# Performance work log

Hardware: AMD Instinct MI355X
Metric: run time of the kernel (lower is better)

## Reference

```python
import jax, jax.numpy as jnp
import numpy as np

ALPHA_LIM = (float(np.exp(-1.0 / 5.0)), float(np.exp(-1.0 / 25.0)))
BETA_LIM = (float(np.exp(-1.0 / 30.0)), float(np.exp(-1.0 / 120.0)))
A_LIM = (-1.0, 1.0)
B_LIM = (0.0, 2.0)
THRESHOLD = 1.0


@jax.custom_vjp
def spike_boxcar(x):
    # Heaviside forward, boxcar surrogate gradient
    return (x > 0).astype(x.dtype)


def _spike_fwd(x):
    return spike_boxcar(x), x


def _spike_bwd(x, g):
    return (jnp.where(jnp.abs(x) <= 0.5, g, jnp.zeros_like(g)),)


spike_boxcar.defvjp(_spike_fwd, _spike_bwd)


def setup_inputs() -> dict:
    key = jax.random.key(0)
    ks = jax.random.split(key, 9)
    B, T, I, H = 128, 512, 512, 512
    return {
        "x": jax.random.normal(ks[0], (B, T, I), dtype=jnp.float32),
        "W": jax.random.normal(ks[1], (H, I), dtype=jnp.float32) / np.sqrt(I),
        "alpha": jax.random.uniform(ks[2], (H,), dtype=jnp.float32),
        "beta": jax.random.uniform(ks[3], (H,), dtype=jnp.float32),
        "a": jax.random.uniform(ks[4], (H,), dtype=jnp.float32),
        "b": jax.random.uniform(ks[5], (H,), dtype=jnp.float32),
        "u0": jax.random.uniform(ks[6], (B, H), dtype=jnp.float32),
        "w0": jax.random.uniform(ks[7], (B, H), dtype=jnp.float32),
        "s0": jax.random.uniform(ks[8], (B, H), dtype=jnp.float32),
    }


def reference(x, W, alpha, beta, a, b, u0, w0, s0):
    # x: [B, T, I]; W: [H, I] (nn.Linear weight, no bias)
    alpha = jnp.clip(alpha, ALPHA_LIM[0], ALPHA_LIM[1])
    beta = jnp.clip(beta, BETA_LIM[0], BETA_LIM[1])
    a = jnp.clip(a, A_LIM[0], A_LIM[1])
    b = jnp.clip(b, B_LIM[0], B_LIM[1])

    Wx = jnp.einsum("bti,hi->bth", x, W)  # [B, T, H]
    Wx_t = jnp.transpose(Wx, (1, 0, 2))    # [T, B, H] for scan over time

    def step(carry, wx_t):
        ut, wt, st = carry
        wt = beta * wt + a * ut + b * st
        ut = alpha * (ut - st) + (1.0 - alpha) * (wx_t - wt)
        st = spike_boxcar(ut - THRESHOLD)
        return (ut, wt, st), st

    _, s = jax.lax.scan(step, (u0, w0, s0), Wx_t)  # s: [T, B, H]
    return jnp.transpose(s, (1, 0, 2))  # [B, T, H]
```

## Files before the change

### kernel.cpp

```cpp
#include <hip/hip_runtime.h>
#include <hip/hip_bf16.h>


#define M_SZ 65536
#define H_SZ 512
#define K_SZ 512
#define B_SZ 128
#define T_SZ 512
#define LSTR 132

typedef __attribute__((ext_vector_type(4))) float f32x4;

__device__ __forceinline__ bool detect_bf16(const unsigned int* __restrict__ w) {
  int c = 0;
#pragma unroll
  for (int i = 0; i < 64; ++i) {
    unsigned int e = (w[i] >> 7) & 0xffu;
    c += (e >= 115u && e <= 131u) ? 1 : 0;
  }
  return c > 32;
}

template <bool ISB>
__device__ __forceinline__ f32x4 ld4t(const void* __restrict__ p, size_t off) {
  if constexpr (!ISB) {
    return *reinterpret_cast<const f32x4*>(reinterpret_cast<const float*>(p) + off);
  } else {
    uint2 v = *reinterpret_cast<const uint2*>(reinterpret_cast<const unsigned short*>(p) + off);
    f32x4 r;
    r.x = __uint_as_float((v.x & 0xffffu) << 16);
    r.y = __uint_as_float(v.x & 0xffff0000u);
    r.z = __uint_as_float((v.y & 0xffffu) << 16);
    r.w = __uint_as_float(v.y & 0xffff0000u);
    return r;
  }
}

template <bool ISB>
__device__ __forceinline__ float ld1t(const void* __restrict__ p, int i) {
  if constexpr (!ISB) return reinterpret_cast<const float*>(p)[i];
  return __uint_as_float((unsigned int)(reinterpret_cast<const unsigned short*>(p)[i]) << 16);
}

__device__ __forceinline__ void gl_lds16(const void* g, void* l) {
  __builtin_amdgcn_global_load_lds(
      (const __attribute__((address_space(1))) void*)g,
      (__attribute__((address_space(3))) void*)l, 16, 0, 0);
}

template <bool ISB>
__device__ __forceinline__ void gemm_body(const void* __restrict__ X,
                                          const void* __restrict__ Wm,
                                          float* __restrict__ C, int mbase,
                                          float* __restrict__ As,
                                          float* __restrict__ Bs) {
  const int tid = threadIdx.x;
  const int r0 = tid >> 2;
  const int q0 = (tid & 3) * 4;
  const int tx = tid & 15;
  const int ty = tid >> 4;
  const size_t M0 = (size_t)mbase + (size_t)(blockIdx.x >> 2) * 128;
  const int N0 = (blockIdx.x & 3) * 128;

  float acc[8][8];
#pragma unroll
  for (int i = 0; i < 8; ++i)
#pragma unroll
    for (int j = 0; j < 8; ++j) acc[i][j] = 0.0f;

  const size_t aoff0 = (M0 + r0) * K_SZ + q0;
  const size_t aoff1 = (M0 + r0 + 64) * K_SZ + q0;
  const size_t boff0 = (size_t)(N0 + r0) * K_SZ + q0;
  const size_t boff1 = (size_t)(N0 + r0 + 64) * K_SZ + q0;

  f32x4 pa0 = ld4t<ISB>(X, aoff0), pa1 = ld4t<ISB>(X, aoff1);
  f32x4 pb0 = ld4t<ISB>(Wm, boff0), pb1 = ld4t<ISB>(Wm, boff1);

  for (int kk = 0; kk < K_SZ; kk += 16) {
    __syncthreads();
    As[(q0 + 0) * LSTR + r0] = pa0.x; As[(q0 + 1) * LSTR + r0] = pa0.y;
    As[(q0 + 2) * LSTR + r0] = pa0.z; As[(q0 + 3) * LSTR + r0] = pa0.w;
    As[(q0 + 0) * LSTR + r0 + 64] = pa1.x; As[(q0 + 1) * LSTR + r0 + 64] = pa1.y;
    As[(q0 + 2) * LSTR + r0 + 64] = pa1.z; As[(q0 + 3) * LSTR + r0 + 64] = pa1.w;
    Bs[(q0 + 0) * LSTR + r0] = pb0.x; Bs[(q0 + 1) * LSTR + r0] = pb0.y;
    Bs[(q0 + 2) * LSTR + r0] = pb0.z; Bs[(q0 + 3) * LSTR + r0] = pb0.w;
    Bs[(q0 + 0) * LSTR + r0 + 64] = pb1.x; Bs[(q0 + 1) * LSTR + r0 + 64] = pb1.y;
    Bs[(q0 + 2) * LSTR + r0 + 64] = pb1.z; Bs[(q0 + 3) * LSTR + r0 + 64] = pb1.w;
    __syncthreads();
    if (kk + 16 < K_SZ) {
      pa0 = ld4t<ISB>(X, aoff0 + kk + 16); pa1 = ld4t<ISB>(X, aoff1 + kk + 16);
      pb0 = ld4t<ISB>(Wm, boff0 + kk + 16); pb1 = ld4t<ISB>(Wm, boff1 + kk + 16);
    }
#pragma unroll
    for (int k = 0; k < 16; ++k) {
      const f32x4 a0 = *reinterpret_cast<const f32x4*>(As + k * LSTR + ty * 4);
      const f32x4 a1 = *reinterpret_cast<const f32x4*>(As + k * LSTR + 64 + ty * 4);
      const f32x4 b0 = *reinterpret_cast<const f32x4*>(Bs + k * LSTR + tx * 4);
      const f32x4 b1 = *reinterpret_cast<const f32x4*>(Bs + k * LSTR + 64 + tx * 4);
      const float av[8] = {a0.x, a0.y, a0.z, a0.w, a1.x, a1.y, a1.z, a1.w};
      const float bv[8] = {b0.x, b0.y, b0.z, b0.w, b1.x, b1.y, b1.z, b1.w};
#pragma unroll
      for (int i = 0; i < 8; ++i)
#pragma unroll
        for (int j = 0; j < 8; ++j) acc[i][j] += av[i] * bv[j];
    }
  }

#pragma unroll
  for (int r = 0; r < 8; ++r) {
    const size_t m = M0 + ((r < 4) ? (ty * 4 + r) : (64 + ty * 4 + (r - 4)));
    float* Cp = C + m * H_SZ + N0;
    f32x4 v0 = {acc[r][0], acc[r][1], acc[r][2], acc[r][3]};
    f32x4 v1 = {acc[r][4], acc[r][5], acc[r][6], acc[r][7]};
    __builtin_nontemporal_store(v0, reinterpret_cast<f32x4*>(Cp + tx * 4));
    __builtin_nontemporal_store(v1, reinterpret_cast<f32x4*>(Cp + 64 + tx * 4));
  }
}

__global__ __launch_bounds__(256) void sgemm_bt(const void* __restrict__ X,
                                                const void* __restrict__ Wm,
                                                float* __restrict__ C, int mbase) {
  __shared__ float As[16 * LSTR];
  __shared__ float Bs[16 * LSTR];
  if (detect_bf16(reinterpret_cast<const unsigned int*>(X)))
    gemm_body<true>(X, Wm, C, mbase, As, Bs);
  else
    gemm_body<false>(X, Wm, C, mbase, As, Bs);
}

#define SCH 16
#define NCH (T_SZ / SCH)
#define NSL 3

template <bool ISB>
__device__ __forceinline__ void scan_body(
    const float* __restrict__ wx, const void* __restrict__ alpha_p,
    const void* __restrict__ beta_p, const void* __restrict__ a_p,
    const void* __restrict__ b_p, const void* __restrict__ u0p,
    const void* __restrict__ w0p, const void* __restrict__ s0p,
    void* __restrict__ out, float* __restrict__ ring) {
  const int lane = threadIdx.x;
  const int b = blockIdx.x >> 3;
  const int strip = blockIdx.x & 7;
  const int h0 = strip * 64;
  const int h = h0 + lane;

  const float al = fminf(fmaxf(ld1t<ISB>(alpha_p, h), (float)0.8187307530779818),
                         (float)0.9607894391523232);
  const float be = fminf(fmaxf(ld1t<ISB>(beta_p, h), (float)0.9672161004820059),
                         (float)0.9917013044213351);
  const float av = fminf(fmaxf(ld1t<ISB>(a_p, h), -1.0f), 1.0f);
  const float bv = fminf(fmaxf(ld1t<ISB>(b_p, h), 0.0f), 2.0f);
  const float om = __fsub_rn(1.0f, al);

  const int bh = b * H_SZ + h;
  float u = ld1t<ISB>(u0p, bh);
  float w = ld1t<ISB>(w0p, bh);
  float s = ld1t<ISB>(s0p, bh);

  const float* xb = wx + (size_t)b * T_SZ * H_SZ + h0;
  float* outf = reinterpret_cast<float*>(out);
  __hip_bfloat16* outb = reinterpret_cast<__hip_bfloat16*>(out);
  const size_t ob0 = (size_t)b * T_SZ * H_SZ + h;

  auto issue = [&](int c) {
    float* dst = ring + (c % NSL) * (SCH * 64);
#pragma unroll
    for (int j = 0; j < 4; ++j) {
      int t = c * SCH + j * 4 + (lane >> 4);
      t = (t < T_SZ) ? t : (T_SZ - 1);
      gl_lds16(xb + (size_t)t * H_SZ + (lane & 15) * 4, dst + j * 256);
    }
  };

  issue(0); issue(1); issue(2);

  for (int c = 0; c < NCH; ++c) {
    if (c == 0)      asm volatile("s_waitcnt vmcnt(8)" ::: "memory");
    else if (c == 1) asm volatile("s_waitcnt vmcnt(24)" ::: "memory");
    else             asm volatile("s_waitcnt vmcnt(40)" ::: "memory");
    const float* cb = ring + (c % NSL) * (SCH * 64);
#pragma unroll
    for (int jt = 0; jt < SCH; ++jt) {
      const float cur = cb[jt * 64 + lane];
      w = __fadd_rn(__fadd_rn(__fmul_rn(be, w), __fmul_rn(av, u)), __fmul_rn(bv, s));
      u = __fadd_rn(__fmul_rn(al, __fsub_rn(u, s)), __fmul_rn(om, __fsub_rn(cur, w)));
      s = (u > 1.0f) ? 1.0f : 0.0f;
      const size_t o = ob0 + (size_t)(c * SCH + jt) * H_SZ;
      if constexpr (ISB) outb[o] = __float2bfloat16(s);
      else outf[o] = s;
    }
    issue(c + 3);
  }
}

__global__ __launch_bounds__(64) void lif_scan(
    const float* __restrict__ wx, const void* __restrict__ X,
    const void* __restrict__ alpha_p, const void* __restrict__ beta_p,
    const void* __restrict__ a_p, const void* __restrict__ b_p,
    const void* __restrict__ u0p, const void* __restrict__ w0p,
    const void* __restrict__ s0p, void* __restrict__ out) {
  __shared__ float ring[NSL * SCH * 64];
  if (detect_bf16(reinterpret_cast<const unsigned int*>(X)))
    scan_body<true>(wx, alpha_p, beta_p, a_p, b_p, u0p, w0p, s0p, out, ring);
  else
    scan_body<false>(wx, alpha_p, beta_p, a_p, b_p, u0p, w0p, s0p, out, ring);
}

extern "C" void kernel_launch(void* const* d_in, const int* in_sizes, int n_in,
                              void* d_out, int out_size, void* d_ws, size_t ws_size,
                              hipStream_t stream) {
  const void* X = d_in[0];
  const void* Wm = d_in[1];
  float* ws = reinterpret_cast<float*>(d_ws);

  for (int q = 0; q < 4; ++q)
    sgemm_bt<<<dim3(512), dim3(256), 0, stream>>>(X, Wm, ws, q * (M_SZ / 4));

  lif_scan<<<dim3(B_SZ * 8), dim3(64), 0, stream>>>(
      ws, X, d_in[2], d_in[3], d_in[4], d_in[5], d_in[6], d_in[7], d_in[8], d_out);
}
```

Measured before the change: 652.8 us.

## Merge GEMM launches into one grid and prefetch scan inputs into registers

The four quarter-sized GEMM launches become a single launch of 2048 blocks, removing per-launch overhead and tail gaps. The scan kernel drops the LDS ring filled by global_load_lds and its manual vmcnt waits. Each lane now loads its own column directly into a register ring of 4 chunks of 8 timesteps, prefetching four chunks ahead. This trades coalesced 16-byte LDS staging for 4-byte per-lane loads, which are still contiguous across the 64-lane wave, and raises register pressure.

```diff
diff --git a/kernel.cpp b/kernel.cpp
--- a/kernel.cpp
+++ b/kernel.cpp
@@ -42,16 +42,10 @@
   return __uint_as_float((unsigned int)(reinterpret_cast<const unsigned short*>(p)[i]) << 16);
 }
 
-__device__ __forceinline__ void gl_lds16(const void* g, void* l) {
-  __builtin_amdgcn_global_load_lds(
-      (const __attribute__((address_space(1))) void*)g,
-      (__attribute__((address_space(3))) void*)l, 16, 0, 0);
-}
-
 template <bool ISB>
 __device__ __forceinline__ void gemm_body(const void* __restrict__ X,
                                           const void* __restrict__ Wm,
-                                          float* __restrict__ C, int mbase,
+                                          float* __restrict__ C,
                                           float* __restrict__ As,
                                           float* __restrict__ Bs) {
   const int tid = threadIdx.x;
@@ -59,7 +53,7 @@
   const int q0 = (tid & 3) * 4;
   const int tx = tid & 15;
   const int ty = tid >> 4;
-  const size_t M0 = (size_t)mbase + (size_t)(blockIdx.x >> 2) * 128;
+  const size_t M0 = (size_t)(blockIdx.x >> 2) * 128;
   const int N0 = (blockIdx.x & 3) * 128;
 
   float acc[8][8];
@@ -119,18 +113,17 @@
 
 __global__ __launch_bounds__(256) void sgemm_bt(const void* __restrict__ X,
                                                 const void* __restrict__ Wm,
-                                                float* __restrict__ C, int mbase) {
+                                                float* __restrict__ C) {
   __shared__ float As[16 * LSTR];
   __shared__ float Bs[16 * LSTR];
   if (detect_bf16(reinterpret_cast<const unsigned int*>(X)))
-    gemm_body<true>(X, Wm, C, mbase, As, Bs);
+    gemm_body<true>(X, Wm, C, As, Bs);
   else
-    gemm_body<false>(X, Wm, C, mbase, As, Bs);
-}
-
-#define SCH 16
-#define NCH (T_SZ / SCH)
-#define NSL 3
+    gemm_body<false>(X, Wm, C, As, Bs);
+}
+
+#define SCT 8
+#define SNC (T_SZ / SCT)
 
 template <bool ISB>
 __device__ __forceinline__ void scan_body(
@@ -138,11 +131,10 @@
     const void* __restrict__ beta_p, const void* __restrict__ a_p,
     const void* __restrict__ b_p, const void* __restrict__ u0p,
     const void* __restrict__ w0p, const void* __restrict__ s0p,
-    void* __restrict__ out, float* __restrict__ ring) {
+    void* __restrict__ out) {
   const int lane = threadIdx.x;
   const int b = blockIdx.x >> 3;
-  const int strip = blockIdx.x & 7;
-  const int h0 = strip * 64;
+  const int h0 = (blockIdx.x & 7) * 64;
   const int h = h0 + lane;
 
   const float al = fminf(fmaxf(ld1t<ISB>(alpha_p, h), (float)0.8187307530779818),
@@ -158,39 +150,39 @@
   float w = ld1t<ISB>(w0p, bh);
   float s = ld1t<ISB>(s0p, bh);
 
-  const float* xb = wx + (size_t)b * T_SZ * H_SZ + h0;
+  const float* xb = wx + (size_t)b * T_SZ * H_SZ + h;
   float* outf = reinterpret_cast<float*>(out);
   __hip_bfloat16* outb = reinterpret_cast<__hip_bfloat16*>(out);
   const size_t ob0 = (size_t)b * T_SZ * H_SZ + h;
 
-  auto issue = [&](int c) {
-    float* dst = ring + (c % NSL) * (SCH * 64);
-#pragma unroll
-    for (int j = 0; j < 4; ++j) {
-      int t = c * SCH + j * 4 + (lane >> 4);
+  float ring[4][SCT];
+  auto loadc = [&](float* dst, int c) {
+#pragma unroll
+    for (int j = 0; j < SCT; ++j) {
+      int t = c * SCT + j;
       t = (t < T_SZ) ? t : (T_SZ - 1);
-      gl_lds16(xb + (size_t)t * H_SZ + (lane & 15) * 4, dst + j * 256);
+      dst[j] = xb[(size_t)t * H_SZ];
     }
   };
 
-  issue(0); issue(1); issue(2);
-
-  for (int c = 0; c < NCH; ++c) {
-    if (c == 0)      asm volatile("s_waitcnt vmcnt(8)" ::: "memory");
-    else if (c == 1) asm volatile("s_waitcnt vmcnt(24)" ::: "memory");
-    else             asm volatile("s_waitcnt vmcnt(40)" ::: "memory");
-    const float* cb = ring + (c % NSL) * (SCH * 64);
-#pragma unroll
-    for (int jt = 0; jt < SCH; ++jt) {
-      const float cur = cb[jt * 64 + lane];
-      w = __fadd_rn(__fadd_rn(__fmul_rn(be, w), __fmul_rn(av, u)), __fmul_rn(bv, s));
-      u = __fadd_rn(__fmul_rn(al, __fsub_rn(u, s)), __fmul_rn(om, __fsub_rn(cur, w)));
-      s = (u > 1.0f) ? 1.0f : 0.0f;
-      const size_t o = ob0 + (size_t)(c * SCH + jt) * H_SZ;
-      if constexpr (ISB) outb[o] = __float2bfloat16(s);
-      else outf[o] = s;
-    }
-    issue(c + 3);
+  loadc(ring[0], 0); loadc(ring[1], 1); loadc(ring[2], 2); loadc(ring[3], 3);
+
+  for (int c0 = 0; c0 < SNC; c0 += 4) {
+#pragma unroll
+    for (int p = 0; p < 4; ++p) {
+      const int c = c0 + p;
+#pragma unroll
+      for (int j = 0; j < SCT; ++j) {
+        const float cur = ring[p][j];
+        w = __fadd_rn(__fadd_rn(__fmul_rn(be, w), __fmul_rn(av, u)), __fmul_rn(bv, s));
+        u = __fadd_rn(__fmul_rn(al, __fsub_rn(u, s)), __fmul_rn(om, __fsub_rn(cur, w)));
+        s = (u > 1.0f) ? 1.0f : 0.0f;
+        const size_t o = ob0 + (size_t)(c * SCT + j) * H_SZ;
+        if constexpr (ISB) outb[o] = __float2bfloat16(s);
+        else outf[o] = s;
+      }
+      loadc(ring[p], c + 4);
+    }
   }
 }
 
@@ -200,11 +192,10 @@
     const void* __restrict__ a_p, const void* __restrict__ b_p,
     const void* __restrict__ u0p, const void* __restrict__ w0p,
     const void* __restrict__ s0p, void* __restrict__ out) {
-  __shared__ float ring[NSL * SCH * 64];
   if (detect_bf16(reinterpret_cast<const unsigned int*>(X)))
-    scan_body<true>(wx, alpha_p, beta_p, a_p, b_p, u0p, w0p, s0p, out, ring);
+    scan_body<true>(wx, alpha_p, beta_p, a_p, b_p, u0p, w0p, s0p, out);
   else
-    scan_body<false>(wx, alpha_p, beta_p, a_p, b_p, u0p, w0p, s0p, out, ring);
+    scan_body<false>(wx, alpha_p, beta_p, a_p, b_p, u0p, w0p, s0p, out);
 }
 
 extern "C" void kernel_launch(void* const* d_in, const int* in_sizes, int n_in,
@@ -214,8 +205,7 @@
   const void* Wm = d_in[1];
   float* ws = reinterpret_cast<float*>(d_ws);
 
-  for (int q = 0; q < 4; ++q)
-    sgemm_bt<<<dim3(512), dim3(256), 0, stream>>>(X, Wm, ws, q * (M_SZ / 4));
+  sgemm_bt<<<dim3((M_SZ / 128) * (H_SZ / 128)), dim3(256), 0, stream>>>(X, Wm, ws);
 
   lif_scan<<<dim3(B_SZ * 8), dim3(64), 0, stream>>>(
       ws, X, d_in[2], d_in[3], d_in[4], d_in[5], d_in[6], d_in[7], d_in[8], d_out);
```

Result: faster. 622.2 us (-4.7%).
